# Optimization experiments

Measured on AMD Instinct MI355X. Metric: run time of the kernel, lower is better.

Reference implementation:

```python
import jax, jax.numpy as jnp
import numpy as np
from math import sqrt

DIM = 256
HEADS = 4
GROUPS = min(DIM // 4, 32)  # = 32
EPS = 1e-6


def setup_inputs() -> dict:
    key = jax.random.key(0)
    ks = jax.random.split(key, 10)
    B, C, H, W = 16, DIM, 32, 32
    x = jax.random.normal(ks[0], (B, C, H, W), dtype=jnp.float32)
    s = 1.0 / sqrt(C)
    inp = {
        'x': x,
        'gn_scale': jnp.ones((C,), jnp.float32),
        'gn_bias': jnp.zeros((C,), jnp.float32),
        'Wq': jax.random.normal(ks[1], (C, C), jnp.float32) * s,
        'bq': jnp.zeros((C,), jnp.float32),
        'Wk': jax.random.normal(ks[2], (C, C), jnp.float32) * s,
        'bk': jnp.zeros((C,), jnp.float32),
        'Wv': jax.random.normal(ks[3], (C, C), jnp.float32) * s,
        'bv': jnp.zeros((C,), jnp.float32),
        'Wp': jax.random.normal(ks[4], (C, C), jnp.float32) * s,
        'bp': jnp.zeros((C,), jnp.float32),
    }
    return inp


def _group_norm(x, scale, bias):
    B, C, H, W = x.shape
    xg = x.reshape(B, GROUPS, C // GROUPS, H, W)
    mean = xg.mean(axis=(2, 3, 4), keepdims=True)
    var = xg.var(axis=(2, 3, 4), keepdims=True)
    xg = (xg - mean) * jax.lax.rsqrt(var + EPS)
    x = xg.reshape(B, C, H, W)
    return x * scale[None, :, None, None] + bias[None, :, None, None]


def _lin_ch(x, W, b):
    # 1x1 conv / linear over channel dim: (B,C,H,W) x (C,Cout) -> (B,Cout,H,W)
    return jnp.einsum('bchw,cd->bdhw', x, W) + b[None, :, None, None]


def reference(x, gn_scale, gn_bias, Wq, bq, Wk, bk, Wv, bv, Wp, bp):
    B, C, H, W = x.shape
    dh = C // HEADS
    _x = _group_norm(x, gn_scale, gn_bias)
    q = _lin_ch(_x, Wq, bq).reshape(B, HEADS, dh, H, W)
    k = _lin_ch(_x, Wk, bk).reshape(B, HEADS, dh, H, W)
    v = _lin_ch(_x, Wv, bv).reshape(B, HEADS, dh, H, W)
    scores = jnp.einsum('bhdxy,bhdij->bhxyij', q, k) / sqrt(C)
    scores = scores.reshape(B, HEADS, H, W, H * W)
    weights = jax.nn.softmax(scores, axis=-1).reshape(B, HEADS, H, W, H, W)
    h = jnp.einsum('bhxyij,bhdij->bhdxy', weights, v).reshape(B, C, H, W)
    h = _lin_ch(h, Wp, bp)
    ret = (x + h) / sqrt(2.0)
    return ret
```

## Files before the change

### kernel.cpp

```cpp
#include <hip/hip_runtime.h>
#include <hip/hip_bf16.h>

#define BATCH 16
#define CH    256
#define HW    1024
#define NH    4
#define DH    64
#define NG    32
#define CPG   8
#define EPSV  1e-6f

#define QSCALE 0.090168440055558706f

typedef __bf16 bf16x8 __attribute__((ext_vector_type(8)));
typedef float  f32x4  __attribute__((ext_vector_type(4)));

__device__ __forceinline__ unsigned short f2bf(float f) {
    union { __hip_bfloat16 h; unsigned short u; } cv;
    cv.h = __float2bfloat16(f);
    return cv.u;
}

__device__ __forceinline__ unsigned int fbits(float f) {
    union { float f; unsigned int u; } cv; cv.f = f; return cv.u;
}

__device__ __forceinline__ void gld_lds16(const unsigned short* g, unsigned short* l) {
    __builtin_amdgcn_global_load_lds(
        (const __attribute__((address_space(1))) void*)g,
        (__attribute__((address_space(3))) void*)l, 16, 0, 0);
}

__global__ void prep_stats_kernel(const float* x, const float* scale, const float* bias,
                                  const float* Wq, const float* Wk, const float* Wv,
                                  const float* Wp, const float* bq, const float* bk,
                                  const float* bv, float* coefA, float* coefB,
                                  unsigned short* wqkv_t, unsigned short* wp_t,
                                  float* bqkv) {
    int t = threadIdx.x;
    if (blockIdx.x >= 512) {
        int idx = (blockIdx.x - 512) * 256 + t;
        if (idx < 768 * 256) {
            int n = idx >> 8, c = idx & 255;
            const float* W = (n < 256) ? Wq : (n < 512) ? Wk : Wv;
            int d = n & 255;
            wqkv_t[idx] = f2bf(W[c * 256 + d]);
        } else if (idx < 768 * 256 + 256 * 256) {
            int j = idx - 768 * 256;
            int n = j >> 8, c = j & 255;
            wp_t[j] = f2bf(Wp[c * 256 + n]);
        }
        if (idx < 768)
            bqkv[idx] = (idx < 256) ? bq[idx] : (idx < 512) ? bk[idx - 256] : bv[idx - 512];
        return;
    }
    int bg = blockIdx.x;
    const float4* p = reinterpret_cast<const float4*>(x + (size_t)bg * (CPG * HW));
    float s = 0.f, ss = 0.f;
    for (int i = t; i < CPG * HW / 4; i += 256) {
        float4 v = p[i];
        s += v.x + v.y + v.z + v.w;
        ss += v.x * v.x + v.y * v.y + v.z * v.z + v.w * v.w;
    }
    for (int o = 32; o; o >>= 1) { s += __shfl_down(s, o); ss += __shfl_down(ss, o); }
    __shared__ float as[4], ass[4];
    int w = t >> 6;
    if ((t & 63) == 0) { as[w] = s; ass[w] = ss; }
    __syncthreads();
    if (t < 8) {
        float S = as[0] + as[1] + as[2] + as[3];
        float SS = ass[0] + ass[1] + ass[2] + ass[3];
        float mean = S / (float)(CPG * HW);
        float var = SS / (float)(CPG * HW) - mean * mean;
        float rstd = rsqrtf(var + EPSV);
        int b = bg >> 5, g = bg & 31;
        int c = g * CPG + t;
        float a = rstd * scale[c];
        coefA[b * CH + c] = a;
        coefB[b * CH + c] = bias[c] - mean * a;
    }
}

__global__ __launch_bounds__(256) void qkv_kernel(const float* x,
        const float* coefA, const float* coefB,
        const unsigned short* wqkv_t, const float* bqkv,
        unsigned short* qb, unsigned short* kb, unsigned short* vb) {
    int t = threadIdx.x;
    int wv = t >> 6, lane = t & 63, quad = lane >> 4, ln = lane & 15;
    int wr = wv >> 1, wc = wv & 1;
    int bx = blockIdx.x;
    int m0 = bx * 128 + wr * 64;
    int n0 = blockIdx.y * 128 + wc * 64;
    int bb = bx >> 3;
    int p0 = (bx & 7) * 128;

    __shared__ __align__(16) unsigned short lds_a[128][40];
    __shared__ __align__(16) float ebuf[4][16][68];

    const float* xb = x + (size_t)bb * CH * HW + p0;
    const float* cA = coefA + bb * CH;
    const float* cB = coefB + bb * CH;

    int sp = t & 127;
    int sbase = (t >> 7) * 2;

    f32x4 acc[4][4] = {};
    for (int k0 = 0; k0 < CH; k0 += 32) {
        bf16x8 wpk[2];
#pragma unroll
        for (int rep = 0; rep < 2; rep++) {
            int s = sbase + rep;
            int cb = k0 + s * 8;
            union { bf16x8 v8; __hip_bfloat162 h2[4]; } u;
#pragma unroll
            for (int j = 0; j < 4; j++) {
                float v0 = fmaf(xb[(size_t)(cb + 2 * j)     * HW + sp], cA[cb + 2 * j],     cB[cb + 2 * j]);
                float v1 = fmaf(xb[(size_t)(cb + 2 * j + 1) * HW + sp], cA[cb + 2 * j + 1], cB[cb + 2 * j + 1]);
                u.h2[j] = __float22bfloat162_rn(float2{v0, v1});
            }
            wpk[rep] = u.v8;
        }
        __syncthreads();
#pragma unroll
        for (int rep = 0; rep < 2; rep++) {
            int s = sbase + rep;
            int phys = s ^ (sp & 3);
            *reinterpret_cast<bf16x8*>(&lds_a[sp][phys * 8]) = wpk[rep];
        }
        __syncthreads();
        bf16x8 af[4], bfr[4];
#pragma unroll
        for (int i = 0; i < 4; i++) {
            int p = wr * 64 + i * 16 + ln;
            af[i] = *reinterpret_cast<const bf16x8*>(&lds_a[p][(quad ^ (p & 3)) * 8]);
        }
#pragma unroll
        for (int j = 0; j < 4; j++)
            bfr[j] = *reinterpret_cast<const bf16x8*>(
                wqkv_t + (size_t)(n0 + j * 16 + ln) * CH + k0 + quad * 8);
#pragma unroll
        for (int i = 0; i < 4; i++)
#pragma unroll
            for (int j = 0; j < 4; j++)
                acc[i][j] = __builtin_amdgcn_mfma_f32_16x16x32_bf16(af[i], bfr[j], acc[i][j], 0, 0, 0);
    }

    int whichw = n0 >> 8;
    int headw = (n0 >> 6) & 3;
    int bi = m0 >> 10;
    int p0w = m0 & 1023;
    int bh = bi * NH + headw;
    float biasj[4];
#pragma unroll
    for (int j = 0; j < 4; j++) biasj[j] = bqkv[n0 + j * 16 + ln];

    if (whichw < 2) {
        unsigned short* dst = (whichw == 0 ? qb : kb) + (size_t)bh * HW * DH;
        float sc = (whichw == 0) ? QSCALE : 1.0f;
#pragma unroll
        for (int i = 0; i < 4; i++) {
#pragma unroll
            for (int j = 0; j < 4; j++)
#pragma unroll
                for (int r = 0; r < 4; r++)
                    ebuf[wv][quad * 4 + r][j * 16 + ln] = (acc[i][j][r] + biasj[j]) * sc;
#pragma unroll
            for (int pg = 0; pg < 2; pg++) {
                int mloc = pg * 8 + quad * 2 + (ln >> 3);
                int dd = (ln & 7) * 8;
                f32x4 a0 = *reinterpret_cast<const f32x4*>(&ebuf[wv][mloc][dd]);
                f32x4 a1 = *reinterpret_cast<const f32x4*>(&ebuf[wv][mloc][dd + 4]);
                union { uint4 u4; unsigned int u[4]; } o;
                union { __hip_bfloat162 h2; unsigned int u; } cv;
                cv.h2 = __float22bfloat162_rn(float2{a0[0], a0[1]}); o.u[0] = cv.u;
                cv.h2 = __float22bfloat162_rn(float2{a0[2], a0[3]}); o.u[1] = cv.u;
                cv.h2 = __float22bfloat162_rn(float2{a1[0], a1[1]}); o.u[2] = cv.u;
                cv.h2 = __float22bfloat162_rn(float2{a1[2], a1[3]}); o.u[3] = cv.u;
                *reinterpret_cast<uint4*>(dst + (size_t)(p0w + i * 16 + mloc) * DH + dd) = o.u4;
            }
        }
    } else {
        unsigned short* dstv = vb + (size_t)bh * DH * HW;
#pragma unroll
        for (int j = 0; j < 4; j++) {
            int d = j * 16 + ln;
#pragma unroll
            for (int i = 0; i < 4; i++) {
                int p = p0w + i * 16 + quad * 4;
                ushort4 pk4;
                pk4.x = f2bf(acc[i][j][0] + biasj[j]);
                pk4.y = f2bf(acc[i][j][1] + biasj[j]);
                pk4.z = f2bf(acc[i][j][2] + biasj[j]);
                pk4.w = f2bf(acc[i][j][3] + biasj[j]);
                *reinterpret_cast<ushort4*>(dstv + (size_t)d * HW + p) = pk4;
            }
        }
    }
}

__global__ __launch_bounds__(256) void attn_kernel(const unsigned short* qb,
        const unsigned short* kb, const unsigned short* vb, unsigned short* h_t) {
    int linear = blockIdx.x;
    int bh = linear & 63;
    int qblk = linear >> 6;
    int t = threadIdx.x;
    int wv = t >> 6, lane = t & 63, quad = lane >> 4, ln = lane & 15;
    int q0 = qblk * 128 + wv * 32;

    const unsigned short* Q = qb + (size_t)bh * HW * DH;
    const unsigned short* K = kb + (size_t)bh * HW * DH;
    const unsigned short* V = vb + (size_t)bh * DH * HW;

    __shared__ __align__(16) unsigned short kbuf[2][4096];
    __shared__ __align__(16) unsigned short vbuf[2][4096];
    __shared__ __align__(16) unsigned short pbuf[4][2][16][72];

    int c_a = wv * 64 + lane;
    int c_b = 256 + wv * 64 + lane;
    int pa = c_a >> 3, ja = (c_a & 7) ^ (pa & 7);
    int pb = c_b >> 3, jb = (c_b & 7) ^ (pb & 7);
    const unsigned short* pka = K + (size_t)pa * DH + ja * 8;
    const unsigned short* pkb = K + (size_t)pb * DH + jb * 8;
    const unsigned short* pva = V + (size_t)pa * HW + ja * 8;
    const unsigned short* pvb = V + (size_t)pb * HW + jb * 8;
    int lofs_a = wv * 512, lofs_b = 2048 + wv * 512;

    int koffs[4][2];
#pragma unroll
    for (int mt = 0; mt < 4; mt++) {
        int p = mt * 16 + ln, sw = p & 7;
#pragma unroll
        for (int kk = 0; kk < 2; kk++)
            koffs[mt][kk] = p * 64 + (((kk * 4 + quad) ^ sw) * 8);
    }

    bf16x8 qf[2][2];
#pragma unroll
    for (int nq = 0; nq < 2; nq++)
#pragma unroll
        for (int kk = 0; kk < 2; kk++)
            qf[nq][kk] = *reinterpret_cast<const bf16x8*>(
                Q + (size_t)(q0 + nq * 16 + ln) * DH + kk * 32 + quad * 8);

    f32x4 ls[2] = {};
    f32x4 o[2][4] = {};

    gld_lds16(pka, &kbuf[0][lofs_a]);
    gld_lds16(pkb, &kbuf[0][lofs_b]);
    gld_lds16(pva, &vbuf[0][lofs_a]);
    gld_lds16(pvb, &vbuf[0][lofs_b]);
    pka += 64 * DH; pkb += 64 * DH; pva += 64; pvb += 64;

#define ATTN_TILE(B, DO_STAGE)                                                      \
    {                                                                               \
        __syncthreads();                                                            \
        if (DO_STAGE) {                                                             \
            gld_lds16(pka, &kbuf[B ^ 1][lofs_a]);                                   \
            gld_lds16(pkb, &kbuf[B ^ 1][lofs_b]);                                   \
            gld_lds16(pva, &vbuf[B ^ 1][lofs_a]);                                   \
            gld_lds16(pvb, &vbuf[B ^ 1][lofs_b]);                                   \
            pka += 64 * DH; pkb += 64 * DH; pva += 64; pvb += 64;                   \
        }                                                                           \
        bf16x8 kf[4][2], vf[4][2];                                                  \
        _Pragma("unroll")                                                           \
        for (int mt = 0; mt < 4; mt++) {                                            \
            _Pragma("unroll")                                                       \
            for (int kk = 0; kk < 2; kk++) {                                        \
                kf[mt][kk] = *reinterpret_cast<const bf16x8*>(&kbuf[B][koffs[mt][kk]]); \
                vf[mt][kk] = *reinterpret_cast<const bf16x8*>(&vbuf[B][koffs[mt][kk]]); \
            }                                                                       \
        }                                                                           \
        f32x4 s[2][4] = {};                                                         \
        _Pragma("unroll")                                                           \
        for (int nq = 0; nq < 2; nq++)                                              \
            _Pragma("unroll")                                                       \
            for (int mt = 0; mt < 4; mt++) {                                        \
                s[nq][mt] = __builtin_amdgcn_mfma_f32_16x16x32_bf16(kf[mt][0], qf[nq][0], s[nq][mt], 0, 0, 0); \
                s[nq][mt] = __builtin_amdgcn_mfma_f32_16x16x32_bf16(kf[mt][1], qf[nq][1], s[nq][mt], 0, 0, 0); \
            }                                                                       \
        _Pragma("unroll")                                                           \
        for (int nq = 0; nq < 2; nq++)                                              \
            _Pragma("unroll")                                                       \
            for (int mt = 0; mt < 4; mt++) {                                        \
                float e0 = __builtin_amdgcn_exp2f(s[nq][mt][0]);                    \
                float e1 = __builtin_amdgcn_exp2f(s[nq][mt][1]);                    \
                float e2 = __builtin_amdgcn_exp2f(s[nq][mt][2]);                    \
                float e3 = __builtin_amdgcn_exp2f(s[nq][mt][3]);                    \
                ls[nq][0] += e0; ls[nq][1] += e1;                                   \
                ls[nq][2] += e2; ls[nq][3] += e3;                                   \
                uint2 pk2;                                                          \
                pk2.x = __builtin_amdgcn_perm(fbits(e1), fbits(e0), 0x07060302u);   \
                pk2.y = __builtin_amdgcn_perm(fbits(e3), fbits(e2), 0x07060302u);   \
                *reinterpret_cast<uint2*>(&pbuf[wv][nq][ln][mt * 16 + quad * 4]) = pk2; \
            }                                                                       \
        _Pragma("unroll")                                                           \
        for (int nq = 0; nq < 2; nq++)                                              \
            _Pragma("unroll")                                                       \
            for (int kk = 0; kk < 2; kk++) {                                        \
                bf16x8 pf = *reinterpret_cast<const bf16x8*>(&pbuf[wv][nq][ln][kk * 32 + quad * 8]); \
                _Pragma("unroll")                                                   \
                for (int mt = 0; mt < 4; mt++)                                      \
                    o[nq][mt] = __builtin_amdgcn_mfma_f32_16x16x32_bf16(vf[mt][kk], pf, o[nq][mt], 0, 0, 0); \
            }                                                                       \
    }

    for (int u = 0; u < 8; u++) {
        ATTN_TILE(0, true)
        ATTN_TILE(1, (u < 7))
    }
#undef ATTN_TILE

    int b_ = bh >> 2, head = bh & 3;
#pragma unroll
    for (int nq = 0; nq < 2; nq++) {
        float lsum = ls[nq][0] + ls[nq][1] + ls[nq][2] + ls[nq][3];
        lsum += __shfl_xor(lsum, 16);
        lsum += __shfl_xor(lsum, 32);
        float inv = 1.0f / lsum;
        unsigned short* dst = h_t + ((size_t)b_ * HW + q0 + nq * 16 + ln) * CH + head * DH;
#pragma unroll
        for (int mt = 0; mt < 4; mt++) {
            ushort4 pk4;
            pk4.x = f2bf(o[nq][mt][0] * inv);
            pk4.y = f2bf(o[nq][mt][1] * inv);
            pk4.z = f2bf(o[nq][mt][2] * inv);
            pk4.w = f2bf(o[nq][mt][3] * inv);
            *reinterpret_cast<ushort4*>(dst + mt * 16 + quad * 4) = pk4;
        }
    }
}

__global__ __launch_bounds__(256) void proj_kernel(const unsigned short* h_t,
        const unsigned short* wp_t, const float* bp, const float* x, float* out) {
    int t = threadIdx.x;
    int wv = t >> 6, lane = t & 63, quad = lane >> 4, ln = lane & 15;
    int m0 = blockIdx.x * 16;
    int n0 = wv * 64;

    f32x4 acc[4] = {};
    for (int k0 = 0; k0 < CH; k0 += 32) {
        int koff = k0 + quad * 8;
        bf16x8 af = *reinterpret_cast<const bf16x8*>(h_t + (size_t)(m0 + ln) * CH + koff);
        bf16x8 bfr[4];
#pragma unroll
        for (int j = 0; j < 4; j++)
            bfr[j] = *reinterpret_cast<const bf16x8*>(wp_t + (size_t)(n0 + j * 16 + ln) * CH + koff);
#pragma unroll
        for (int j = 0; j < 4; j++)
            acc[j] = __builtin_amdgcn_mfma_f32_16x16x32_bf16(af, bfr[j], acc[j], 0, 0, 0);
    }
    const float inv_s2 = 0.70710678118654752440f;
    int mb = m0 + quad * 4;
    int bi = mb >> 10, p = mb & 1023;
#pragma unroll
    for (int j = 0; j < 4; j++) {
        int n = n0 + j * 16 + ln;
        float bias = bp[n];
        size_t off = ((size_t)(bi * CH + n)) * HW + p;
        float4 xv = *reinterpret_cast<const float4*>(x + off);
        float4 ov;
        ov.x = (xv.x + acc[j][0] + bias) * inv_s2;
        ov.y = (xv.y + acc[j][1] + bias) * inv_s2;
        ov.z = (xv.z + acc[j][2] + bias) * inv_s2;
        ov.w = (xv.w + acc[j][3] + bias) * inv_s2;
        *reinterpret_cast<float4*>(out + off) = ov;
    }
}

extern "C" void kernel_launch(void* const* d_in, const int* in_sizes, int n_in,
                              void* d_out, int out_size, void* d_ws, size_t ws_size,
                              hipStream_t stream) {
    const float* x        = (const float*)d_in[0];
    const float* gn_scale = (const float*)d_in[1];
    const float* gn_bias  = (const float*)d_in[2];
    const float* Wq = (const float*)d_in[3];
    const float* bq = (const float*)d_in[4];
    const float* Wk = (const float*)d_in[5];
    const float* bk = (const float*)d_in[6];
    const float* Wv = (const float*)d_in[7];
    const float* bv = (const float*)d_in[8];
    const float* Wp = (const float*)d_in[9];
    const float* bp = (const float*)d_in[10];
    float* out = (float*)d_out;

    char* ws = (char*)d_ws;
    float*          bqkv   = (float*)(ws + 0);
    float*          coefA  = (float*)(ws + 4096);
    float*          coefB  = (float*)(ws + 20480);
    unsigned short* wqkv_t = (unsigned short*)(ws + 36864);
    unsigned short* wp_t   = (unsigned short*)(ws + 430080);
    unsigned short* h_t    = (unsigned short*)(ws + 1048576);
    unsigned short* qb     = (unsigned short*)(ws + 9437184);
    unsigned short* kb     = (unsigned short*)(ws + 17825792);
    unsigned short* vb     = (unsigned short*)(ws + 26214400);

    prep_stats_kernel<<<1536, 256, 0, stream>>>(x, gn_scale, gn_bias, Wq, Wk, Wv, Wp,
                                                bq, bk, bv, coefA, coefB, wqkv_t, wp_t, bqkv);
    qkv_kernel<<<dim3(128, 6), 256, 0, stream>>>(x, coefA, coefB, wqkv_t, bqkv, qb, kb, vb);
    attn_kernel<<<512, 256, 0, stream>>>(qb, kb, vb, h_t);
    proj_kernel<<<dim3(1024, 1), 256, 0, stream>>>(h_t, wp_t, bp, x, out);
}
```

Measured before the change: 162.7 us.

## Double-buffer and prefetch QKV GEMM inputs; halve attention query tile per wave

In the QKV kernel, the next k-step's x values are prefetched into registers and the A tile is double-buffered in LDS, which removes one barrier per iteration. The epilogue buffer now aliases the same shared memory, and occupancy is hinted with launch_bounds(256,3). The attention kernel now handles 16 queries per wave instead of 32 and launches twice as many blocks, trading more K/V reloads for more parallelism and fewer registers per thread.

```diff
diff --git a/kernel.cpp b/kernel.cpp
--- a/kernel.cpp
+++ b/kernel.cpp
@@ -81,7 +81,7 @@
     }
 }
 
-__global__ __launch_bounds__(256) void qkv_kernel(const float* x,
+__global__ __launch_bounds__(256, 3) void qkv_kernel(const float* x,
         const float* coefA, const float* coefB,
         const unsigned short* wqkv_t, const float* bqkv,
         unsigned short* qb, unsigned short* kb, unsigned short* vb) {
@@ -94,8 +94,10 @@
     int bb = bx >> 3;
     int p0 = (bx & 7) * 128;
 
-    __shared__ __align__(16) unsigned short lds_a[128][40];
-    __shared__ __align__(16) float ebuf[4][16][68];
+    __shared__ __align__(16) char smem[20480];
+    typedef unsigned short ldsa_row[40];
+    ldsa_row* lds_a0 = reinterpret_cast<ldsa_row*>(smem);
+    ldsa_row* lds_a1 = reinterpret_cast<ldsa_row*>(smem + 10240);
 
     const float* xb = x + (size_t)bb * CH * HW + p0;
     const float* cA = coefA + bb * CH;
@@ -103,36 +105,47 @@
 
     int sp = t & 127;
     int sbase = (t >> 7) * 2;
+    int c0t = sbase * 8;
+    const float* xcol = xb + sp;
+
+    float cur[16], nxt[16];
+#pragma unroll
+    for (int c = 0; c < 16; c++) cur[c] = xcol[(size_t)(c0t + c) * HW];
 
     f32x4 acc[4][4] = {};
-    for (int k0 = 0; k0 < CH; k0 += 32) {
+    for (int it = 0; it < 8; it++) {
+        int k0 = it * 32;
         bf16x8 wpk[2];
 #pragma unroll
         for (int rep = 0; rep < 2; rep++) {
-            int s = sbase + rep;
-            int cb = k0 + s * 8;
             union { bf16x8 v8; __hip_bfloat162 h2[4]; } u;
 #pragma unroll
             for (int j = 0; j < 4; j++) {
-                float v0 = fmaf(xb[(size_t)(cb + 2 * j)     * HW + sp], cA[cb + 2 * j],     cB[cb + 2 * j]);
-                float v1 = fmaf(xb[(size_t)(cb + 2 * j + 1) * HW + sp], cA[cb + 2 * j + 1], cB[cb + 2 * j + 1]);
+                int c = rep * 8 + 2 * j;
+                int cg = k0 + c0t + c;
+                float v0 = fmaf(cur[c],     cA[cg],     cB[cg]);
+                float v1 = fmaf(cur[c + 1], cA[cg + 1], cB[cg + 1]);
                 u.h2[j] = __float22bfloat162_rn(float2{v0, v1});
             }
             wpk[rep] = u.v8;
         }
-        __syncthreads();
+        ldsa_row* la = (it & 1) ? lds_a1 : lds_a0;
 #pragma unroll
         for (int rep = 0; rep < 2; rep++) {
             int s = sbase + rep;
             int phys = s ^ (sp & 3);
-            *reinterpret_cast<bf16x8*>(&lds_a[sp][phys * 8]) = wpk[rep];
+            *reinterpret_cast<bf16x8*>(&la[sp][phys * 8]) = wpk[rep];
         }
         __syncthreads();
         bf16x8 af[4], bfr[4];
 #pragma unroll
         for (int i = 0; i < 4; i++) {
             int p = wr * 64 + i * 16 + ln;
-            af[i] = *reinterpret_cast<const bf16x8*>(&lds_a[p][(quad ^ (p & 3)) * 8]);
+            af[i] = *reinterpret_cast<const bf16x8*>(&la[p][(quad ^ (p & 3)) * 8]);
+        }
+        if (it < 7) {
+#pragma unroll
+            for (int c = 0; c < 16; c++) nxt[c] = xcol[(size_t)(k0 + 32 + c0t + c) * HW];
         }
 #pragma unroll
         for (int j = 0; j < 4; j++)
@@ -143,7 +156,14 @@
 #pragma unroll
             for (int j = 0; j < 4; j++)
                 acc[i][j] = __builtin_amdgcn_mfma_f32_16x16x32_bf16(af[i], bfr[j], acc[i][j], 0, 0, 0);
-    }
+        if (it < 7) {
+#pragma unroll
+            for (int c = 0; c < 16; c++) cur[c] = nxt[c];
+        }
+    }
+
+    __syncthreads();
+    float* ebw = reinterpret_cast<float*>(smem) + wv * (16 * 68);
 
     int whichw = n0 >> 8;
     int headw = (n0 >> 6) & 3;
@@ -163,13 +183,13 @@
             for (int j = 0; j < 4; j++)
 #pragma unroll
                 for (int r = 0; r < 4; r++)
-                    ebuf[wv][quad * 4 + r][j * 16 + ln] = (acc[i][j][r] + biasj[j]) * sc;
+                    ebw[(quad * 4 + r) * 68 + j * 16 + ln] = (acc[i][j][r] + biasj[j]) * sc;
 #pragma unroll
             for (int pg = 0; pg < 2; pg++) {
                 int mloc = pg * 8 + quad * 2 + (ln >> 3);
                 int dd = (ln & 7) * 8;
-                f32x4 a0 = *reinterpret_cast<const f32x4*>(&ebuf[wv][mloc][dd]);
-                f32x4 a1 = *reinterpret_cast<const f32x4*>(&ebuf[wv][mloc][dd + 4]);
+                f32x4 a0 = *reinterpret_cast<const f32x4*>(&ebw[mloc * 68 + dd]);
+                f32x4 a1 = *reinterpret_cast<const f32x4*>(&ebw[mloc * 68 + dd + 4]);
                 union { uint4 u4; unsigned int u[4]; } o;
                 union { __hip_bfloat162 h2; unsigned int u; } cv;
                 cv.h2 = __float22bfloat162_rn(float2{a0[0], a0[1]}); o.u[0] = cv.u;
@@ -205,7 +225,7 @@
     int qblk = linear >> 6;
     int t = threadIdx.x;
     int wv = t >> 6, lane = t & 63, quad = lane >> 4, ln = lane & 15;
-    int q0 = qblk * 128 + wv * 32;
+    int q0 = qblk * 64 + wv * 16;
 
     const unsigned short* Q = qb + (size_t)bh * HW * DH;
     const unsigned short* K = kb + (size_t)bh * HW * DH;
@@ -213,7 +233,7 @@
 
     __shared__ __align__(16) unsigned short kbuf[2][4096];
     __shared__ __align__(16) unsigned short vbuf[2][4096];
-    __shared__ __align__(16) unsigned short pbuf[4][2][16][72];
+    __shared__ __align__(16) unsigned short pbuf[4][16][72];
 
     int c_a = wv * 64 + lane;
     int c_b = 256 + wv * 64 + lane;
@@ -234,16 +254,14 @@
             koffs[mt][kk] = p * 64 + (((kk * 4 + quad) ^ sw) * 8);
     }
 
-    bf16x8 qf[2][2];
-#pragma unroll
-    for (int nq = 0; nq < 2; nq++)
-#pragma unroll
-        for (int kk = 0; kk < 2; kk++)
-            qf[nq][kk] = *reinterpret_cast<const bf16x8*>(
-                Q + (size_t)(q0 + nq * 16 + ln) * DH + kk * 32 + quad * 8);
-
-    f32x4 ls[2] = {};
-    f32x4 o[2][4] = {};
+    bf16x8 qf[2];
+#pragma unroll
+    for (int kk = 0; kk < 2; kk++)
+        qf[kk] = *reinterpret_cast<const bf16x8*>(
+            Q + (size_t)(q0 + ln) * DH + kk * 32 + quad * 8);
+
+    f32x4 ls = {0.f, 0.f, 0.f, 0.f};
+    f32x4 o[4] = {};
 
     gld_lds16(pka, &kbuf[0][lofs_a]);
     gld_lds16(pkb, &kbuf[0][lofs_b]);
@@ -270,38 +288,31 @@
                 vf[mt][kk] = *reinterpret_cast<const bf16x8*>(&vbuf[B][koffs[mt][kk]]); \
             }                                                                       \
         }                                                                           \
-        f32x4 s[2][4] = {};                                                         \
+        f32x4 s[4] = {};                                                            \
         _Pragma("unroll")                                                           \
-        for (int nq = 0; nq < 2; nq++)                                              \
+        for (int mt = 0; mt < 4; mt++) {                                            \
+            s[mt] = __builtin_amdgcn_mfma_f32_16x16x32_bf16(kf[mt][0], qf[0], s[mt], 0, 0, 0); \
+            s[mt] = __builtin_amdgcn_mfma_f32_16x16x32_bf16(kf[mt][1], qf[1], s[mt], 0, 0, 0); \
+        }                                                                           \
+        _Pragma("unroll")                                                           \
+        for (int mt = 0; mt < 4; mt++) {                                            \
+            float e0 = __builtin_amdgcn_exp2f(s[mt][0]);                            \
+            float e1 = __builtin_amdgcn_exp2f(s[mt][1]);                            \
+            float e2 = __builtin_amdgcn_exp2f(s[mt][2]);                            \
+            float e3 = __builtin_amdgcn_exp2f(s[mt][3]);                            \
+            ls[0] += e0; ls[1] += e1; ls[2] += e2; ls[3] += e3;                     \
+            uint2 pk2;                                                              \
+            pk2.x = __builtin_amdgcn_perm(fbits(e1), fbits(e0), 0x07060302u);       \
+            pk2.y = __builtin_amdgcn_perm(fbits(e3), fbits(e2), 0x07060302u);       \
+            *reinterpret_cast<uint2*>(&pbuf[wv][ln][mt * 16 + quad * 4]) = pk2;     \
+        }                                                                           \
+        _Pragma("unroll")                                                           \
+        for (int kk = 0; kk < 2; kk++) {                                            \
+            bf16x8 pf = *reinterpret_cast<const bf16x8*>(&pbuf[wv][ln][kk * 32 + quad * 8]); \
             _Pragma("unroll")                                                       \
-            for (int mt = 0; mt < 4; mt++) {                                        \
-                s[nq][mt] = __builtin_amdgcn_mfma_f32_16x16x32_bf16(kf[mt][0], qf[nq][0], s[nq][mt], 0, 0, 0); \
-                s[nq][mt] = __builtin_amdgcn_mfma_f32_16x16x32_bf16(kf[mt][1], qf[nq][1], s[nq][mt], 0, 0, 0); \
-            }                                                                       \
-        _Pragma("unroll")                                                           \
-        for (int nq = 0; nq < 2; nq++)                                              \
-            _Pragma("unroll")                                                       \
-            for (int mt = 0; mt < 4; mt++) {                                        \
-                float e0 = __builtin_amdgcn_exp2f(s[nq][mt][0]);                    \
-                float e1 = __builtin_amdgcn_exp2f(s[nq][mt][1]);                    \
-                float e2 = __builtin_amdgcn_exp2f(s[nq][mt][2]);                    \
-                float e3 = __builtin_amdgcn_exp2f(s[nq][mt][3]);                    \
-                ls[nq][0] += e0; ls[nq][1] += e1;                                   \
-                ls[nq][2] += e2; ls[nq][3] += e3;                                   \
-                uint2 pk2;                                                          \
-                pk2.x = __builtin_amdgcn_perm(fbits(e1), fbits(e0), 0x07060302u);   \
-                pk2.y = __builtin_amdgcn_perm(fbits(e3), fbits(e2), 0x07060302u);   \
-                *reinterpret_cast<uint2*>(&pbuf[wv][nq][ln][mt * 16 + quad * 4]) = pk2; \
-            }                                                                       \
-        _Pragma("unroll")                                                           \
-        for (int nq = 0; nq < 2; nq++)                                              \
-            _Pragma("unroll")                                                       \
-            for (int kk = 0; kk < 2; kk++) {                                        \
-                bf16x8 pf = *reinterpret_cast<const bf16x8*>(&pbuf[wv][nq][ln][kk * 32 + quad * 8]); \
-                _Pragma("unroll")                                                   \
-                for (int mt = 0; mt < 4; mt++)                                      \
-                    o[nq][mt] = __builtin_amdgcn_mfma_f32_16x16x32_bf16(vf[mt][kk], pf, o[nq][mt], 0, 0, 0); \
-            }                                                                       \
+            for (int mt = 0; mt < 4; mt++)                                          \
+                o[mt] = __builtin_amdgcn_mfma_f32_16x16x32_bf16(vf[mt][kk], pf, o[mt], 0, 0, 0); \
+        }                                                                           \
     }
 
     for (int u = 0; u < 8; u++) {
@@ -311,22 +322,19 @@
 #undef ATTN_TILE
 
     int b_ = bh >> 2, head = bh & 3;
-#pragma unroll
-    for (int nq = 0; nq < 2; nq++) {
-        float lsum = ls[nq][0] + ls[nq][1] + ls[nq][2] + ls[nq][3];
-        lsum += __shfl_xor(lsum, 16);
-        lsum += __shfl_xor(lsum, 32);
-        float inv = 1.0f / lsum;
-        unsigned short* dst = h_t + ((size_t)b_ * HW + q0 + nq * 16 + ln) * CH + head * DH;
-#pragma unroll
-        for (int mt = 0; mt < 4; mt++) {
-            ushort4 pk4;
-            pk4.x = f2bf(o[nq][mt][0] * inv);
-            pk4.y = f2bf(o[nq][mt][1] * inv);
-            pk4.z = f2bf(o[nq][mt][2] * inv);
-            pk4.w = f2bf(o[nq][mt][3] * inv);
-            *reinterpret_cast<ushort4*>(dst + mt * 16 + quad * 4) = pk4;
-        }
+    float lsum = ls[0] + ls[1] + ls[2] + ls[3];
+    lsum += __shfl_xor(lsum, 16);
+    lsum += __shfl_xor(lsum, 32);
+    float inv = 1.0f / lsum;
+    unsigned short* dst = h_t + ((size_t)b_ * HW + q0 + ln) * CH + head * DH;
+#pragma unroll
+    for (int mt = 0; mt < 4; mt++) {
+        ushort4 pk4;
+        pk4.x = f2bf(o[mt][0] * inv);
+        pk4.y = f2bf(o[mt][1] * inv);
+        pk4.z = f2bf(o[mt][2] * inv);
+        pk4.w = f2bf(o[mt][3] * inv);
+        *reinterpret_cast<ushort4*>(dst + mt * 16 + quad * 4) = pk4;
     }
 }
 
@@ -397,6 +405,6 @@
     prep_stats_kernel<<<1536, 256, 0, stream>>>(x, gn_scale, gn_bias, Wq, Wk, Wv, Wp,
                                                 bq, bk, bv, coefA, coefB, wqkv_t, wp_t, bqkv);
     qkv_kernel<<<dim3(128, 6), 256, 0, stream>>>(x, coefA, coefB, wqkv_t, bqkv, qb, kb, vb);
-    attn_kernel<<<512, 256, 0, stream>>>(qb, kb, vb, h_t);
+    attn_kernel<<<1024, 256, 0, stream>>>(qb, kb, vb, h_t);
     proj_kernel<<<dim3(1024, 1), 256, 0, stream>>>(h_t, wp_t, bp, x, out);
 }
```

After: 200.9 us. 23.5% more time.
